# Performance work log

Measured on AMD Instinct MI355X. Metric: run time of the kernel, lower is better.

## Reference

```python
import jax, jax.numpy as jnp
import numpy as np

B, INDIM, POSDIM, L, H, DE, DV, RECEPT = 2, 256, 256, 2048, 8, 64, 64, 64
LN_EPS = 1e-5


def pos_embedding(dim, length):
    # sin/cos with geometric wavelengths length/(0.8 + 1.2**(i+1)); shape (dim, length)
    dsin = dim // 2
    dcos = dim - dsin
    sin_wl = length / (0.8 + 1.2 ** (jnp.arange(dsin, dtype=jnp.float32) + 1.0))[:, None]
    cos_wl = length / (0.8 + 1.2 ** (jnp.arange(dcos, dtype=jnp.float32) + 1.0))[:, None]
    xpos = jnp.arange(length, dtype=jnp.float32)[None, :]
    two_pi = 2.0 * np.pi
    return jnp.concatenate([jnp.sin(two_pi * xpos / sin_wl), jnp.cos(two_pi * xpos / cos_wl)], axis=0)


def _layernorm(x, g, b):
    # normalize over last axis
    mu = jnp.mean(x, axis=-1, keepdims=True)
    var = jnp.mean((x - mu) ** 2, axis=-1, keepdims=True)
    return (x - mu) / jnp.sqrt(var + LN_EPS) * g + b


def setup_inputs() -> dict:
    key = jax.random.key(0)
    ks = jax.random.split(key, 10)
    s = 0.02
    inp = {
        "x": jax.random.normal(ks[0], (B, INDIM, L), dtype=jnp.float32),
        "Wq": jax.random.normal(ks[1], (H * DE, INDIM + POSDIM), dtype=jnp.float32) * s,
        "Wk": jax.random.normal(ks[2], (H * DE, INDIM + POSDIM), dtype=jnp.float32) * s,
        "Wv": jax.random.normal(ks[3], (H * DV, INDIM + POSDIM), dtype=jnp.float32) * s,
        "Wres": jax.random.normal(ks[4], (DV, INDIM), dtype=jnp.float32) * s,
        "Wc": jax.random.normal(ks[5], (DV, H * DV), dtype=jnp.float32) * s,
        "ln1_g": jnp.ones((DV,), jnp.float32),
        "ln1_b": jnp.zeros((DV,), jnp.float32),
        "W1": jax.random.normal(ks[6], (4 * DV, DV), dtype=jnp.float32) * s,
        "W2": jax.random.normal(ks[7], (DV, 4 * DV), dtype=jnp.float32) * s,
        "ln2_g": jnp.ones((DV,), jnp.float32),
        "ln2_b": jnp.zeros((DV,), jnp.float32),
    }
    return inp


def reference(x, Wq, Wk, Wv, Wres, Wc, ln1_g, ln1_b, W1, W2, ln2_g, ln2_b):
    bsz = x.shape[0]
    # residual projection (1x1 conv == channel matmul)
    residual = jnp.einsum('oi,bil->bol', Wres, x)
    # concat positional embedding along channel dim
    pos = pos_embedding(POSDIM, L)
    xp = jnp.concatenate([x, jnp.broadcast_to(pos[None], (bsz,) + pos.shape)], axis=1)
    # QKV projections -> (B, H, D, L)
    q = jnp.einsum('oi,bil->bol', Wq, xp).reshape(bsz, H, DE, L)
    k = jnp.einsum('oi,bil->bol', Wk, xp).reshape(bsz, H, DE, L)
    v = jnp.einsum('oi,bil->bol', Wv, xp).reshape(bsz, H, DV, L)
    # banded receptive attention: mask*(Q^T K); out-of-band scores are exactly 0 (NOT -inf),
    # matching sum(q.unsqueeze(-2) * mask * k.unsqueeze(-3), -1)
    idx = jnp.arange(L)
    band = (jnp.abs(idx[:, None] - idx[None, :]) <= RECEPT).astype(x.dtype)  # (L, L)
    scores = jnp.einsum('bhdl,bhdm->bhlm', q, k) * band / np.float32(np.sqrt(DE))
    attn = jax.nn.softmax(scores, axis=-1)
    # attn @ V^T, back to (B, H, DV, L), flatten heads
    out = jnp.einsum('bhlm,bhvm->bhvl', attn, v).reshape(bsz, H * DV, L)
    pred = jnp.einsum('oi,bil->bol', Wc, out) + residual
    pred = _layernorm(pred.transpose(0, 2, 1), ln1_g, ln1_b).transpose(0, 2, 1)
    # feedforward (1x1 convs) with exact GELU + residual + layernorm
    res2 = pred
    h = jax.nn.gelu(jnp.einsum('oi,bil->bol', W1, pred), approximate=False)
    pred = jnp.einsum('oi,bil->bol', W2, h) + res2
    pred = _layernorm(pred.transpose(0, 2, 1), ln2_g, ln2_b).transpose(0, 2, 1)
    return pred
```

## Files before the change

kernel.cpp:

```cpp
#include <hip/hip_runtime.h>
#include <cstdint>
#include <cstddef>

#define SEQLEN 2048
#define NBATCH 2
#define NIND   256
#define NPOS   256
#define NCIN   512
#define NH     8
#define NDE    64
#define NDV    64
#define NREC   64

typedef __attribute__((ext_vector_type(8))) short s16x8;
typedef __attribute__((ext_vector_type(4))) float f32x4;

__device__ __forceinline__ unsigned short f2bf(float f) {
  union { float f; unsigned u; } v; v.f = f;
  unsigned r = v.u + 0x7fffu + ((v.u >> 16) & 1u);
  return (unsigned short)(r >> 16);
}

__device__ __forceinline__ void gload16(const unsigned short* g, unsigned short* l) {
  __builtin_amdgcn_global_load_lds(
      (const __attribute__((address_space(1))) unsigned int*)g,
      (__attribute__((address_space(3))) unsigned int*)l, 16, 0, 0);
}

__global__ __launch_bounds__(256) void prep_k(const float* __restrict__ x,
                                              const float* __restrict__ Wq,
                                              const float* __restrict__ Wk,
                                              const float* __restrict__ Wv,
                                              const float* __restrict__ Wc,
                                              const float* __restrict__ Wres,
                                              const float* __restrict__ W1,
                                              const float* __restrict__ W2,
                                              unsigned short* __restrict__ xpt,
                                              unsigned short* __restrict__ wqb,
                                              unsigned short* __restrict__ wkb,
                                              unsigned short* __restrict__ wvb,
                                              unsigned short* __restrict__ wcb,
                                              unsigned short* __restrict__ wresb,
                                              unsigned short* __restrict__ w1b,
                                              unsigned short* __restrict__ w2b,
                                              float* __restrict__ vsum) {
  __shared__ float tile[64][65];
  int blk = blockIdx.x;
  int t = threadIdx.x;
  if (blk < 512) {
    int b = blk >> 8, c0 = ((blk >> 5) & 7) * 64, l0 = (blk & 31) * 64;
    if (c0 < NIND) {
      const float* src = x + ((size_t)b * NIND + c0) * SEQLEN;
      int ll = t & 63, cq = t >> 6;
#pragma unroll
      for (int i = 0; i < 16; ++i) {
        int cl = cq * 16 + i;
        tile[cl][ll] = src[(size_t)cl * SEQLEN + l0 + ll];
      }
      __syncthreads();
      int cl2 = t & 63, lq = t >> 6;
      unsigned short* dst = xpt + ((size_t)b * SEQLEN + l0) * NCIN + c0;
#pragma unroll
      for (int i = 0; i < 16; ++i) {
        int l = lq * 16 + i;
        dst[(size_t)l * NCIN + cl2] = f2bf(tile[cl2][l]);
      }
    } else {
      if (b == 1) return;
      int c = c0 + (t & 63);
      int j = c - NIND;
      int i = (j < NPOS / 2) ? j : j - NPOS / 2;
      const double base = (double)1.2f;
      double p = 1.0;
      for (int tt = 0; tt <= i; ++tt) p *= base;
      float w = 0.8f + (float)p;
      float swl = (float)SEQLEN / w;
      const float two_pi = (float)(2.0 * 3.14159265358979323846);
      int wv = t >> 6;
      unsigned short* dst0 = xpt;
      unsigned short* dst1 = xpt + (size_t)SEQLEN * NCIN;
#pragma unroll
      for (int it = 0; it < 16; ++it) {
        int l = l0 + 16 * wv + it;
        float arg = (two_pi * (float)l) / swl;
        unsigned short val = f2bf((j < NPOS / 2) ? sinf(arg) : cosf(arg));
        dst0[(size_t)l * NCIN + c] = val;
        dst1[(size_t)l * NCIN + c] = val;
      }
    }
  } else if (blk == 1360) {
    ((float4*)vsum)[t] = make_float4(0.f, 0.f, 0.f, 0.f);
  } else {
    const float* in;
    unsigned short* out;
    int idx4;
    if (blk < 1280) {
      int i = (blk - 512) * 256 + t;
      int which = i >> 16;
      idx4 = i & 65535;
      in = (which == 0) ? Wq : ((which == 1) ? Wk : Wv);
      out = (which == 0) ? wqb : ((which == 1) ? wkb : wvb);
    } else if (blk < 1312) { in = Wc;   out = wcb;   idx4 = (blk - 1280) * 256 + t; }
    else if (blk < 1328)   { in = Wres; out = wresb; idx4 = (blk - 1312) * 256 + t; }
    else if (blk < 1344)   { in = W1;   out = w1b;   idx4 = (blk - 1328) * 256 + t; }
    else                   { in = W2;   out = w2b;   idx4 = (blk - 1344) * 256 + t; }
    float4 v = ((const float4*)in)[idx4];
    ((ushort4*)out)[idx4] = make_ushort4(f2bf(v.x), f2bf(v.y), f2bf(v.z), f2bf(v.w));
  }
}

__global__ __launch_bounds__(256) void qkv_gemm_k(const unsigned short* __restrict__ Wqb,
                                                  const unsigned short* __restrict__ Wkb,
                                                  const unsigned short* __restrict__ Wvb,
                                                  const unsigned short* __restrict__ xpt,
                                                  unsigned short* __restrict__ qt,
                                                  unsigned short* __restrict__ kt,
                                                  unsigned short* __restrict__ vb,
                                                  float* __restrict__ vsum) {
  __shared__ alignas(16) unsigned short lds[24576];

  int bz = blockIdx.z;
  int y = blockIdx.y;
  int ysel = y >> 3;
  int m0 = (y & 7) * 64;
  int n0 = blockIdx.x * 128;
  const unsigned short* W = (ysel == 0) ? Wqb : ((ysel == 1) ? Wkb : Wvb);
  const unsigned short* Bg = xpt + (size_t)bz * SEQLEN * NCIN;

  int t = threadIdx.x;
  int w = t >> 6, lane = t & 63, lr = lane & 15, hi = lane >> 4;
  int wm = w >> 1, wn = w & 1;

  int sr = lane >> 3;
  int scs = ((lane & 7) ^ sr) * 8;
  const unsigned short* gA0 = W  + (size_t)(m0 + 16 * w + sr) * 512 + scs;
  const unsigned short* gB0 = Bg + (size_t)(n0 + 32 * w + sr) * 512 + scs;

  int swz = (lr & 7) << 3;

  f32x4 acc[2][4];
#pragma unroll
  for (int i = 0; i < 2; ++i)
#pragma unroll
    for (int j = 0; j < 4; ++j) acc[i][j] = (f32x4){0.f, 0.f, 0.f, 0.f};

  auto stage = [&](int buf, int k0) {
    unsigned short* Ad = lds + buf * 12288 + (16 * w) * 64;
    unsigned short* Bd = lds + buf * 12288 + 4096 + (32 * w) * 64;
    gload16(gA0 + k0,            Ad);
    gload16(gA0 + k0 + 8 * 512,  Ad + 8 * 64);
    gload16(gB0 + k0,            Bd);
    gload16(gB0 + k0 + 8 * 512,  Bd + 8 * 64);
    gload16(gB0 + k0 + 16 * 512, Bd + 16 * 64);
    gload16(gB0 + k0 + 24 * 512, Bd + 24 * 64);
  };
  auto compute = [&](int buf) {
    const unsigned short* Ar = lds + buf * 12288;
    const unsigned short* Br = Ar + 4096;
#pragma unroll
    for (int ks = 0; ks < 2; ++ks) {
      s16x8 af[2], bfv[4];
#pragma unroll
      for (int mt = 0; mt < 2; ++mt)
        af[mt] = *(const s16x8*)&Ar[(32 * wm + 16 * mt + lr) * 64 + ((32 * ks + 8 * hi) ^ swz)];
#pragma unroll
      for (int nt = 0; nt < 4; ++nt)
        bfv[nt] = *(const s16x8*)&Br[(64 * wn + 16 * nt + lr) * 64 + ((32 * ks + 8 * hi) ^ swz)];
#pragma unroll
      for (int mt = 0; mt < 2; ++mt)
#pragma unroll
        for (int nt = 0; nt < 4; ++nt)
          acc[mt][nt] = __builtin_amdgcn_mfma_f32_16x16x32_bf16(af[mt], bfv[nt], acc[mt][nt], 0, 0, 0);
    }
  };

  stage(0, 0);
  stage(1, 64);
#pragma unroll
  for (int it = 0; it < 8; ++it) {
    if (it < 7) {
      asm volatile("s_waitcnt vmcnt(6)" ::: "memory");
    } else {
      asm volatile("s_waitcnt vmcnt(0)" ::: "memory");
    }
    __builtin_amdgcn_s_barrier();
    compute(it & 1);
    __builtin_amdgcn_s_barrier();
    if (it < 6) stage(it & 1, (it + 2) * 64);
  }
  __syncthreads();

  if (ysel == 2) {
#pragma unroll
    for (int mt = 0; mt < 2; ++mt)
#pragma unroll
      for (int reg = 0; reg < 4; ++reg) {
        float p = acc[mt][0][reg] + acc[mt][1][reg] + acc[mt][2][reg] + acc[mt][3][reg];
        p += __shfl_xor(p, 1, 64);
        p += __shfl_xor(p, 2, 64);
        p += __shfl_xor(p, 4, 64);
        p += __shfl_xor(p, 8, 64);
        if (lr == 0)
          atomicAdd(&vsum[bz * 512 + m0 + 32 * wm + 16 * mt + 4 * hi + reg], p);
      }
  }

  if (ysel < 2) {
    unsigned short* Cl = lds;
#pragma unroll
    for (int mt = 0; mt < 2; ++mt)
#pragma unroll
      for (int nt = 0; nt < 4; ++nt) {
        int lloc = 64 * wn + 16 * nt + lr;
        int d0 = 32 * wm + 16 * mt + 4 * hi;
        *(ushort4*)&Cl[lloc * 68 + d0] = make_ushort4(f2bf(acc[mt][nt][0]), f2bf(acc[mt][nt][1]),
                                                      f2bf(acc[mt][nt][2]), f2bf(acc[mt][nt][3]));
      }
    __syncthreads();
    int h = m0 >> 6;
    unsigned short* Cb = ((ysel == 0) ? qt : kt) + ((size_t)(bz * NH + h) * SEQLEN + n0) * 64;
    int rr = t >> 1, cc = (t & 1) * 32;
#pragma unroll
    for (int j = 0; j < 4; ++j)
      *(int4*)&Cb[(size_t)rr * 64 + cc + 8 * j] = *(const int4*)&Cl[rr * 68 + cc + 8 * j];
  } else {
    unsigned short* Cl2 = lds;
#pragma unroll
    for (int mt = 0; mt < 2; ++mt)
#pragma unroll
      for (int nt = 0; nt < 4; ++nt) {
        int lloc = 64 * wn + 16 * nt + lr;
#pragma unroll
        for (int reg = 0; reg < 4; ++reg)
          Cl2[(32 * wm + 16 * mt + 4 * hi + reg) * 132 + lloc] = f2bf(acc[mt][nt][reg]);
      }
    __syncthreads();
    int dd = t >> 2, cc = (t & 3) * 32;
    unsigned short* Vb = vb + ((size_t)(bz * 512 + m0 + dd)) * SEQLEN + n0;
#pragma unroll
    for (int j = 0; j < 4; ++j)
      *(int4*)&Vb[cc + 8 * j] = *(const int4*)&Cl2[dd * 132 + cc + 8 * j];
  }
}

__global__ __launch_bounds__(64) void attn_k(const unsigned short* __restrict__ qt,
                                             const unsigned short* __restrict__ kt,
                                             const unsigned short* __restrict__ vb,
                                             const float* __restrict__ vsum,
                                             unsigned short* __restrict__ attnt) {
  __shared__ alignas(16) unsigned short Ps[16][168];
  __shared__ float rowcoef[16];

  int bz = blockIdx.z, hh = blockIdx.y;
  int l0 = blockIdx.x * 16;
  int bh = bz * NH + hh;
  const unsigned short* Qb = qt + (size_t)bh * SEQLEN * 64;
  const unsigned short* Kb = kt + (size_t)bh * SEQLEN * 64;
  const unsigned short* Vp = vb + (size_t)(bz * 512 + hh * 64) * SEQLEN;
  int vsbase = bz * 512 + hh * 64;

  int t = threadIdx.x;
  int lr = t & 15, hi = t >> 4;

  s16x8 a0 = *(const s16x8*)(Qb + ((size_t)(l0 + lr)) * 64 + 8 * hi);
  s16x8 a1 = *(const s16x8*)(Qb + ((size_t)(l0 + lr)) * 64 + 32 + 8 * hi);

  f32x4 sc[9];
#pragma unroll
  for (int ct = 0; ct < 9; ++ct) {
    int m = l0 - 64 + 16 * ct + lr;
    const unsigned short* kp = Kb + (ptrdiff_t)m * 64;
    s16x8 b0 = *(const s16x8*)(kp + 8 * hi);
    s16x8 b1 = *(const s16x8*)(kp + 32 + 8 * hi);
    f32x4 acc = {0.f, 0.f, 0.f, 0.f};
    acc = __builtin_amdgcn_mfma_f32_16x16x32_bf16(a0, b0, acc, 0, 0, 0);
    acc = __builtin_amdgcn_mfma_f32_16x16x32_bf16(a1, b1, acc, 0, 0, 0);
    sc[ct] = acc;
  }

  float rcv[4];
#pragma unroll
  for (int i = 0; i < 4; ++i) {
    int r = 4 * hi + i;
    int l = l0 + r;
    float mx = 0.0f;
    float sv[9];
#pragma unroll
    for (int ct = 0; ct < 9; ++ct) {
      int c = 16 * ct + lr;
      int m = l0 - 64 + c;
      bool ib = (c >= r) && (c <= r + 128) && (m >= 0) && (m < SEQLEN);
      float s = sc[ct][i] * 0.125f;
      sv[ct] = ib ? s : -1e30f;
      mx = ib ? fmaxf(mx, s) : mx;
    }
    mx = fmaxf(mx, __shfl_xor(mx, 1, 64));
    mx = fmaxf(mx, __shfl_xor(mx, 2, 64));
    mx = fmaxf(mx, __shfl_xor(mx, 4, 64));
    mx = fmaxf(mx, __shfl_xor(mx, 8, 64));
    float e0 = expf(-mx);
    float zs = 0.f;
#pragma unroll
    for (int ct = 0; ct < 9; ++ct) {
      float e = (sv[ct] > -1e29f) ? expf(sv[ct] - mx) : 0.0f;
      sv[ct] = e;
      zs += e;
    }
    zs += __shfl_xor(zs, 1, 64);
    zs += __shfl_xor(zs, 2, 64);
    zs += __shfl_xor(zs, 4, 64);
    zs += __shfl_xor(zs, 8, 64);
    int lo = l - NREC; if (lo < 0) lo = 0;
    int hi2 = l + NREC; if (hi2 > SEQLEN - 1) hi2 = SEQLEN - 1;
    float inv = 1.0f / (zs + (float)(SEQLEN - (hi2 - lo + 1)) * e0);
    rcv[i] = e0 * inv;
#pragma unroll
    for (int ct = 0; ct < 9; ++ct)
      sc[ct][i] = (sv[ct] > 0.0f) ? (sv[ct] - e0) * inv : 0.0f;
  }

#pragma unroll
  for (int i = 0; i < 4; ++i) {
    int r = 4 * hi + i;
#pragma unroll
    for (int ct = 0; ct < 9; ++ct)
      Ps[r][16 * ct + lr] = f2bf(sc[ct][i]);
  }
  for (int z = t; z < 16 * 24; z += 64) Ps[z / 24][144 + z % 24] = 0;
  if (lr == 0) {
#pragma unroll
    for (int i = 0; i < 4; ++i) rowcoef[4 * hi + i] = rcv[i];
  }
  __syncthreads();

  float rcf = rowcoef[lr];
  unsigned short* Ob = attnt + ((size_t)bz * SEQLEN + l0 + lr) * 512 + hh * 64;
#pragma unroll
  for (int vt = 0; vt < 4; ++vt) {
    f32x4 acc = {0.f, 0.f, 0.f, 0.f};
#pragma unroll
    for (int ks = 0; ks < 5; ++ks) {
      int m8 = l0 - 64 + 32 * ks + 8 * hi;
      s16x8 av = *(const s16x8*)(Vp + (ptrdiff_t)(16 * vt + lr) * SEQLEN + m8);
      s16x8 b = *(const s16x8*)&Ps[lr][32 * ks + 8 * hi];
      acc = __builtin_amdgcn_mfma_f32_16x16x32_bf16(av, b, acc, 0, 0, 0);
    }
    float vsv[4];
#pragma unroll
    for (int reg = 0; reg < 4; ++reg) vsv[reg] = vsum[vsbase + 16 * vt + 4 * hi + reg];
    ushort4 o = make_ushort4(f2bf(acc[0] + rcf * vsv[0]), f2bf(acc[1] + rcf * vsv[1]),
                             f2bf(acc[2] + rcf * vsv[2]), f2bf(acc[3] + rcf * vsv[3]));
    *(ushort4*)&Ob[16 * vt + 4 * hi] = o;
  }
}

__global__ __launch_bounds__(64) void tail_k(const unsigned short* __restrict__ wcb,
                                             const unsigned short* __restrict__ wresb,
                                             const unsigned short* __restrict__ w1b,
                                             const unsigned short* __restrict__ w2b,
                                             const unsigned short* __restrict__ attnt,
                                             const unsigned short* __restrict__ xpt,
                                             const float* __restrict__ g1v,
                                             const float* __restrict__ b1v,
                                             const float* __restrict__ g2v,
                                             const float* __restrict__ b2v,
                                             float* __restrict__ outp) {
  __shared__ float gs1[64], bs1[64], gs2[64], bs2[64];
  __shared__ alignas(16) unsigned short pw[16][72];
  __shared__ alignas(16) unsigned short hw[16][264];

  int b = blockIdx.y;
  int l0 = blockIdx.x * 16;
  int t = threadIdx.x;
  int lr = t & 15, hi = t >> 4;
  gs1[t] = g1v[t]; bs1[t] = b1v[t]; gs2[t] = g2v[t]; bs2[t] = b2v[t];
  __syncthreads();

  int lloc = lr;
  const unsigned short* brow = attnt + ((size_t)b * SEQLEN + l0 + lloc) * 512;
  const unsigned short* xrow = xpt + ((size_t)b * SEQLEN + l0 + lloc) * 512;

  f32x4 acc[4];
#pragma unroll
  for (int i = 0; i < 4; ++i) acc[i] = (f32x4){0.f, 0.f, 0.f, 0.f};
#pragma unroll
  for (int ks = 0; ks < 16; ++ks) {
    s16x8 bf = *(const s16x8*)(brow + 32 * ks + 8 * hi);
#pragma unroll
    for (int mt = 0; mt < 4; ++mt) {
      s16x8 af = *(const s16x8*)(wcb + (size_t)(16 * mt + lr) * 512 + 32 * ks + 8 * hi);
      acc[mt] = __builtin_amdgcn_mfma_f32_16x16x32_bf16(af, bf, acc[mt], 0, 0, 0);
    }
  }
#pragma unroll
  for (int ks = 0; ks < 8; ++ks) {
    s16x8 bf = *(const s16x8*)(xrow + 32 * ks + 8 * hi);
#pragma unroll
    for (int mt = 0; mt < 4; ++mt) {
      s16x8 af = *(const s16x8*)(wresb + (size_t)(16 * mt + lr) * 256 + 32 * ks + 8 * hi);
      acc[mt] = __builtin_amdgcn_mfma_f32_16x16x32_bf16(af, bf, acc[mt], 0, 0, 0);
    }
  }
  float resid[4][4];
  {
    float sum = 0.f, sq = 0.f;
#pragma unroll
    for (int mt = 0; mt < 4; ++mt)
#pragma unroll
      for (int reg = 0; reg < 4; ++reg) { float v = acc[mt][reg]; sum += v; sq += v * v; }
    sum += __shfl_xor(sum, 16, 64); sq += __shfl_xor(sq, 16, 64);
    sum += __shfl_xor(sum, 32, 64); sq += __shfl_xor(sq, 32, 64);
    float mu = sum * (1.0f / 64.0f);
    float var = sq * (1.0f / 64.0f) - mu * mu;
    float rstd = rsqrtf(var + 1e-5f);
#pragma unroll
    for (int mt = 0; mt < 4; ++mt) {
      float o[4];
#pragma unroll
      for (int reg = 0; reg < 4; ++reg) {
        int m = 16 * mt + 4 * hi + reg;
        o[reg] = (acc[mt][reg] - mu) * rstd * gs1[m] + bs1[m];
        resid[mt][reg] = o[reg];
      }
      *(ushort4*)&pw[lr][16 * mt + 4 * hi] =
          make_ushort4(f2bf(o[0]), f2bf(o[1]), f2bf(o[2]), f2bf(o[3]));
    }
  }
  __syncthreads();

  {
    s16x8 bf0 = *(const s16x8*)&pw[lr][8 * hi];
    s16x8 bf1 = *(const s16x8*)&pw[lr][32 + 8 * hi];
#pragma unroll
    for (int mt = 0; mt < 16; ++mt) {
      s16x8 a0 = *(const s16x8*)(w1b + (size_t)(16 * mt + lr) * 64 + 8 * hi);
      s16x8 a1 = *(const s16x8*)(w1b + (size_t)(16 * mt + lr) * 64 + 32 + 8 * hi);
      f32x4 a2 = {0.f, 0.f, 0.f, 0.f};
      a2 = __builtin_amdgcn_mfma_f32_16x16x32_bf16(a0, bf0, a2, 0, 0, 0);
      a2 = __builtin_amdgcn_mfma_f32_16x16x32_bf16(a1, bf1, a2, 0, 0, 0);
      float v0 = a2[0], v1 = a2[1], v2 = a2[2], v3 = a2[3];
      v0 = 0.5f * v0 * (1.0f + erff(v0 * 0.70710678118654752440f));
      v1 = 0.5f * v1 * (1.0f + erff(v1 * 0.70710678118654752440f));
      v2 = 0.5f * v2 * (1.0f + erff(v2 * 0.70710678118654752440f));
      v3 = 0.5f * v3 * (1.0f + erff(v3 * 0.70710678118654752440f));
      *(ushort4*)&hw[lr][16 * mt + 4 * hi] = make_ushort4(f2bf(v0), f2bf(v1), f2bf(v2), f2bf(v3));
    }
  }
  __syncthreads();

  f32x4 acc3[4];
#pragma unroll
  for (int i = 0; i < 4; ++i) acc3[i] = (f32x4){0.f, 0.f, 0.f, 0.f};
#pragma unroll
  for (int ks = 0; ks < 8; ++ks) {
    s16x8 bf = *(const s16x8*)&hw[lr][32 * ks + 8 * hi];
#pragma unroll
    for (int mt = 0; mt < 4; ++mt) {
      s16x8 af = *(const s16x8*)(w2b + (size_t)(16 * mt + lr) * 256 + 32 * ks + 8 * hi);
      acc3[mt] = __builtin_amdgcn_mfma_f32_16x16x32_bf16(af, bf, acc3[mt], 0, 0, 0);
    }
  }
#pragma unroll
  for (int mt = 0; mt < 4; ++mt)
#pragma unroll
    for (int reg = 0; reg < 4; ++reg) acc3[mt][reg] += resid[mt][reg];
  float sum = 0.f, sq = 0.f;
#pragma unroll
  for (int mt = 0; mt < 4; ++mt)
#pragma unroll
    for (int reg = 0; reg < 4; ++reg) { float v = acc3[mt][reg]; sum += v; sq += v * v; }
  sum += __shfl_xor(sum, 16, 64); sq += __shfl_xor(sq, 16, 64);
  sum += __shfl_xor(sum, 32, 64); sq += __shfl_xor(sq, 32, 64);
  float mu = sum * (1.0f / 64.0f);
  float var = sq * (1.0f / 64.0f) - mu * mu;
  float rstd = rsqrtf(var + 1e-5f);
  float* ob = outp + (size_t)b * 64 * SEQLEN;
  int l = l0 + lloc;
#pragma unroll
  for (int mt = 0; mt < 4; ++mt)
#pragma unroll
    for (int reg = 0; reg < 4; ++reg) {
      int m = 16 * mt + 4 * hi + reg;
      ob[(size_t)m * SEQLEN + l] = (acc3[mt][reg] - mu) * rstd * gs2[m] + bs2[m];
    }
}

extern "C" void kernel_launch(void* const* d_in, const int* in_sizes, int n_in,
                              void* d_out, int out_size, void* d_ws, size_t ws_size,
                              hipStream_t stream) {
  const float* x    = (const float*)d_in[0];
  const float* Wq   = (const float*)d_in[1];
  const float* Wk   = (const float*)d_in[2];
  const float* Wv   = (const float*)d_in[3];
  const float* Wres = (const float*)d_in[4];
  const float* Wc   = (const float*)d_in[5];
  const float* ln1g = (const float*)d_in[6];
  const float* ln1b = (const float*)d_in[7];
  const float* W1   = (const float*)d_in[8];
  const float* W2   = (const float*)d_in[9];
  const float* ln2g = (const float*)d_in[10];
  const float* ln2b = (const float*)d_in[11];

  char* base = (char*)d_ws;
  unsigned short* xpt   = (unsigned short*)base; base += (size_t)2097152 * 2;
  unsigned short* wqb   = (unsigned short*)base; base += (size_t)262144 * 2;
  unsigned short* wkb   = (unsigned short*)base; base += (size_t)262144 * 2;
  unsigned short* wvb   = (unsigned short*)base; base += (size_t)262144 * 2;
  unsigned short* wcb   = (unsigned short*)base; base += (size_t)32768 * 2;
  unsigned short* wresb = (unsigned short*)base; base += (size_t)16384 * 2;
  unsigned short* w1b   = (unsigned short*)base; base += (size_t)16384 * 2;
  unsigned short* w2b   = (unsigned short*)base; base += (size_t)16384 * 2;
  unsigned short* qt    = (unsigned short*)base; base += (size_t)2097152 * 2;
  unsigned short* kt    = (unsigned short*)base; base += (size_t)2097152 * 2;
  unsigned short* vbb   = (unsigned short*)base; base += (size_t)2097152 * 2;
  float* vsum           = (float*)base;          base += (size_t)1024 * 4;
  unsigned short* attnt = (unsigned short*)base; base += (size_t)2097152 * 2;
  float* outp = (float*)d_out;

  prep_k<<<1361, 256, 0, stream>>>(x, Wq, Wk, Wv, Wc, Wres, W1, W2,
                                   xpt, wqb, wkb, wvb, wcb, wresb, w1b, w2b, vsum);
  qkv_gemm_k<<<dim3(16, 24, NBATCH), 256, 0, stream>>>(wqb, wkb, wvb, xpt, qt, kt, vbb, vsum);
  attn_k<<<dim3(128, NH, NBATCH), 64, 0, stream>>>(qt, kt, vbb, vsum, attnt);
  tail_k<<<dim3(128, NBATCH), 64, 0, stream>>>(wcb, wresb, w1b, w2b, attnt, xpt,
                                               ln1g, ln1b, ln2g, ln2b, outp);
}
```

Before: 70.61 us.

## Fuse attention and tail kernels into one cooperative launch with grid sync

Merges the banded attention kernel and the tail projection/FFN/LayerNorm kernel into a single cooperative kernel. Persistent blocks loop over the attention units and then over the tail units, with a grid-wide barrier between the two phases. The aim is to remove one kernel launch and the inter-kernel gap. In exchange it adds grid-sync overhead and limits the grid to the occupancy-derived block count, with the old two-kernel path kept as a fallback if the cooperative launch fails.

```diff
diff --git a/kernel.cpp b/kernel.cpp
--- a/kernel.cpp
+++ b/kernel.cpp
@@ -1,6 +1,9 @@
 #include <hip/hip_runtime.h>
+#include <hip/hip_cooperative_groups.h>
 #include <cstdint>
 #include <cstddef>
+
+namespace cg = cooperative_groups;
 
 #define SEQLEN 2048
 #define NBATCH 2
@@ -243,23 +246,22 @@
   }
 }
 
-__global__ __launch_bounds__(64) void attn_k(const unsigned short* __restrict__ qt,
-                                             const unsigned short* __restrict__ kt,
-                                             const unsigned short* __restrict__ vb,
-                                             const float* __restrict__ vsum,
-                                             unsigned short* __restrict__ attnt) {
-  __shared__ alignas(16) unsigned short Ps[16][168];
-  __shared__ float rowcoef[16];
-
-  int bz = blockIdx.z, hh = blockIdx.y;
-  int l0 = blockIdx.x * 16;
+
+__device__ __forceinline__ void attn_unit_w(
+    int u, int t, void* smem,
+    const unsigned short* qt, const unsigned short* kt,
+    const unsigned short* vb, const float* vsum, unsigned short* attnt) {
+  unsigned short (*Ps)[168] = (unsigned short(*)[168])smem;
+  float* rowcoef = (float*)((char*)smem + 5376);
+
+  int bz = u >> 10, hh = (u >> 7) & 7;
+  int l0 = (u & 127) * 16;
   int bh = bz * NH + hh;
   const unsigned short* Qb = qt + (size_t)bh * SEQLEN * 64;
   const unsigned short* Kb = kt + (size_t)bh * SEQLEN * 64;
   const unsigned short* Vp = vb + (size_t)(bz * 512 + hh * 64) * SEQLEN;
   int vsbase = bz * 512 + hh * 64;
 
-  int t = threadIdx.x;
   int lr = t & 15, hi = t >> 4;
 
   s16x8 a0 = *(const s16x8*)(Qb + ((size_t)(l0 + lr)) * 64 + 8 * hi);
@@ -354,31 +356,28 @@
   }
 }
 
-__global__ __launch_bounds__(64) void tail_k(const unsigned short* __restrict__ wcb,
-                                             const unsigned short* __restrict__ wresb,
-                                             const unsigned short* __restrict__ w1b,
-                                             const unsigned short* __restrict__ w2b,
-                                             const unsigned short* __restrict__ attnt,
-                                             const unsigned short* __restrict__ xpt,
-                                             const float* __restrict__ g1v,
-                                             const float* __restrict__ b1v,
-                                             const float* __restrict__ g2v,
-                                             const float* __restrict__ b2v,
-                                             float* __restrict__ outp) {
-  __shared__ float gs1[64], bs1[64], gs2[64], bs2[64];
-  __shared__ alignas(16) unsigned short pw[16][72];
-  __shared__ alignas(16) unsigned short hw[16][264];
-
-  int b = blockIdx.y;
-  int l0 = blockIdx.x * 16;
-  int t = threadIdx.x;
+__device__ __forceinline__ void tail_unit_w(
+    int u, int t, void* smem,
+    const unsigned short* wcb, const unsigned short* wresb,
+    const unsigned short* w1b, const unsigned short* w2b,
+    const unsigned short* attnt, const unsigned short* xpt,
+    const float* g1v, const float* b1v, const float* g2v, const float* b2v,
+    float* outp) {
+  float* gs1 = (float*)smem;
+  float* bs1 = gs1 + 64;
+  float* gs2 = bs1 + 64;
+  float* bs2 = gs2 + 64;
+  unsigned short (*pw)[72]  = (unsigned short(*)[72])((char*)smem + 1024);
+  unsigned short (*hw)[264] = (unsigned short(*)[264])((char*)smem + 3328);
+
+  int b = u >> 7;
+  int l0 = (u & 127) * 16;
   int lr = t & 15, hi = t >> 4;
   gs1[t] = g1v[t]; bs1[t] = b1v[t]; gs2[t] = g2v[t]; bs2[t] = b2v[t];
   __syncthreads();
 
-  int lloc = lr;
-  const unsigned short* brow = attnt + ((size_t)b * SEQLEN + l0 + lloc) * 512;
-  const unsigned short* xrow = xpt + ((size_t)b * SEQLEN + l0 + lloc) * 512;
+  const unsigned short* brow = attnt + ((size_t)b * SEQLEN + l0 + lr) * 512;
+  const unsigned short* xrow = xpt + ((size_t)b * SEQLEN + l0 + lr) * 512;
 
   f32x4 acc[4];
 #pragma unroll
@@ -475,7 +474,7 @@
   float var = sq * (1.0f / 64.0f) - mu * mu;
   float rstd = rsqrtf(var + 1e-5f);
   float* ob = outp + (size_t)b * 64 * SEQLEN;
-  int l = l0 + lloc;
+  int l = l0 + lr;
 #pragma unroll
   for (int mt = 0; mt < 4; ++mt)
 #pragma unroll
@@ -483,6 +482,62 @@
       int m = 16 * mt + 4 * hi + reg;
       ob[(size_t)m * SEQLEN + l] = (acc3[mt][reg] - mu) * rstd * gs2[m] + bs2[m];
     }
+}
+
+__global__ __launch_bounds__(64) void attn_tail_k(
+    const unsigned short* __restrict__ qt, const unsigned short* __restrict__ kt,
+    const unsigned short* __restrict__ vb, const float* __restrict__ vsum,
+    unsigned short* __restrict__ attnt,
+    const unsigned short* __restrict__ wcb, const unsigned short* __restrict__ wresb,
+    const unsigned short* __restrict__ w1b, const unsigned short* __restrict__ w2b,
+    const unsigned short* __restrict__ xpt,
+    const float* __restrict__ g1v, const float* __restrict__ b1v,
+    const float* __restrict__ g2v, const float* __restrict__ b2v,
+    float* __restrict__ outp) {
+  __shared__ alignas(16) unsigned char smem[11776];
+  int t = threadIdx.x;
+  int bid = blockIdx.x, nb = gridDim.x;
+
+  for (int u = bid; u < 2048; u += nb) {
+    __syncthreads();
+    attn_unit_w(u, t, smem, qt, kt, vb, vsum, attnt);
+  }
+  __threadfence();
+  cg::this_grid().sync();
+  __threadfence();
+
+  for (int u = bid; u < NBATCH * 128; u += nb) {
+    __syncthreads();
+    tail_unit_w(u, t, smem, wcb, wresb, w1b, w2b, attnt, xpt,
+                g1v, b1v, g2v, b2v, outp);
+  }
+}
+
+__global__ __launch_bounds__(64) void attn_k(const unsigned short* __restrict__ qt,
+                                             const unsigned short* __restrict__ kt,
+                                             const unsigned short* __restrict__ vb,
+                                             const float* __restrict__ vsum,
+                                             unsigned short* __restrict__ attnt) {
+  __shared__ alignas(16) unsigned char smem[5440];
+  int u = ((blockIdx.z * NH + blockIdx.y) << 7) | blockIdx.x;
+  attn_unit_w(u, threadIdx.x, smem, qt, kt, vb, vsum, attnt);
+}
+
+__global__ __launch_bounds__(64) void tail_k(const unsigned short* __restrict__ wcb,
+                                             const unsigned short* __restrict__ wresb,
+                                             const unsigned short* __restrict__ w1b,
+                                             const unsigned short* __restrict__ w2b,
+                                             const unsigned short* __restrict__ attnt,
+                                             const unsigned short* __restrict__ xpt,
+                                             const float* __restrict__ g1v,
+                                             const float* __restrict__ b1v,
+                                             const float* __restrict__ g2v,
+                                             const float* __restrict__ b2v,
+                                             float* __restrict__ outp) {
+  __shared__ alignas(16) unsigned char smem[11776];
+  int u = (blockIdx.y << 7) | blockIdx.x;
+  tail_unit_w(u, threadIdx.x, smem, wcb, wresb, w1b, w2b, attnt, xpt,
+              g1v, b1v, g2v, b2v, outp);
 }
 
 extern "C" void kernel_launch(void* const* d_in, const int* in_sizes, int n_in,
@@ -520,7 +575,25 @@
   prep_k<<<1361, 256, 0, stream>>>(x, Wq, Wk, Wv, Wc, Wres, W1, W2,
                                    xpt, wqb, wkb, wvb, wcb, wresb, w1b, w2b, vsum);
   qkv_gemm_k<<<dim3(16, 24, NBATCH), 256, 0, stream>>>(wqb, wkb, wvb, xpt, qt, kt, vbb, vsum);
-  attn_k<<<dim3(128, NH, NBATCH), 64, 0, stream>>>(qt, kt, vbb, vsum, attnt);
-  tail_k<<<dim3(128, NBATCH), 64, 0, stream>>>(wcb, wresb, w1b, w2b, attnt, xpt,
-                                               ln1g, ln1b, ln2g, ln2b, outp);
-}
+
+  int maxb = 0;
+  hipError_t qerr = hipOccupancyMaxActiveBlocksPerMultiprocessor(&maxb, attn_tail_k, 64, 0);
+  int grid = 0;
+  if (qerr == hipSuccess && maxb > 0) {
+    grid = maxb * 256;
+    if (grid > 2048) grid = 2048;
+  }
+  hipError_t lerr = hipErrorUnknown;
+  if (grid > 0) {
+    void* args[] = {(void*)&qt, (void*)&kt, (void*)&vbb, (void*)&vsum, (void*)&attnt,
+                    (void*)&wcb, (void*)&wresb, (void*)&w1b, (void*)&w2b, (void*)&xpt,
+                    (void*)&ln1g, (void*)&ln1b, (void*)&ln2g, (void*)&ln2b, (void*)&outp};
+    lerr = hipLaunchCooperativeKernel((const void*)attn_tail_k, dim3(grid), dim3(64),
+                                      args, 0, stream);
+  }
+  if (lerr != hipSuccess) {
+    attn_k<<<dim3(128, NH, NBATCH), 64, 0, stream>>>(qt, kt, vbb, vsum, attnt);
+    tail_k<<<dim3(128, NBATCH), 64, 0, stream>>>(wcb, wresb, w1b, w2b, attnt, xpt,
+                                                 ln1g, ln1b, ln2g, ln2b, outp);
+  }
+}
```

New measurement: 72.66 us. 1.03x slower.

## Fuse banded attention into tail kernel, keep per-tile attention output in LDS

Applied to the files above, without the earlier changes.

Merges the attention kernel and the output-projection/FFN tail kernel into a single kernel. Each 16-position block loops over all 8 heads and writes the attention output into a shared-memory tile, which then feeds the Wc projection directly. This removes one kernel launch and the round trip of the attention output through global memory. In exchange, the attention grid drops from 2048 single-wave blocks to 256, and each block processes the heads serially. That cuts the parallelism and latency hiding available to the attention phase.

```diff
diff --git a/kernel.cpp b/kernel.cpp
--- a/kernel.cpp
+++ b/kernel.cpp
@@ -243,149 +243,136 @@
   }
 }
 
-__global__ __launch_bounds__(64) void attn_k(const unsigned short* __restrict__ qt,
-                                             const unsigned short* __restrict__ kt,
-                                             const unsigned short* __restrict__ vb,
-                                             const float* __restrict__ vsum,
-                                             unsigned short* __restrict__ attnt) {
+#define ALP 520
+__global__ __launch_bounds__(64) void attn_tail_k(
+    const unsigned short* __restrict__ qt, const unsigned short* __restrict__ kt,
+    const unsigned short* __restrict__ vb, const float* __restrict__ vsum,
+    const unsigned short* __restrict__ wcb, const unsigned short* __restrict__ wresb,
+    const unsigned short* __restrict__ w1b, const unsigned short* __restrict__ w2b,
+    const unsigned short* __restrict__ xpt,
+    const float* __restrict__ g1v, const float* __restrict__ b1v,
+    const float* __restrict__ g2v, const float* __restrict__ b2v,
+    float* __restrict__ outp) {
+  __shared__ alignas(16) unsigned short attn_loc[16][ALP];
   __shared__ alignas(16) unsigned short Ps[16][168];
   __shared__ float rowcoef[16];
-
-  int bz = blockIdx.z, hh = blockIdx.y;
-  int l0 = blockIdx.x * 16;
-  int bh = bz * NH + hh;
-  const unsigned short* Qb = qt + (size_t)bh * SEQLEN * 64;
-  const unsigned short* Kb = kt + (size_t)bh * SEQLEN * 64;
-  const unsigned short* Vp = vb + (size_t)(bz * 512 + hh * 64) * SEQLEN;
-  int vsbase = bz * 512 + hh * 64;
-
-  int t = threadIdx.x;
-  int lr = t & 15, hi = t >> 4;
-
-  s16x8 a0 = *(const s16x8*)(Qb + ((size_t)(l0 + lr)) * 64 + 8 * hi);
-  s16x8 a1 = *(const s16x8*)(Qb + ((size_t)(l0 + lr)) * 64 + 32 + 8 * hi);
-
-  f32x4 sc[9];
-#pragma unroll
-  for (int ct = 0; ct < 9; ++ct) {
-    int m = l0 - 64 + 16 * ct + lr;
-    const unsigned short* kp = Kb + (ptrdiff_t)m * 64;
-    s16x8 b0 = *(const s16x8*)(kp + 8 * hi);
-    s16x8 b1 = *(const s16x8*)(kp + 32 + 8 * hi);
-    f32x4 acc = {0.f, 0.f, 0.f, 0.f};
-    acc = __builtin_amdgcn_mfma_f32_16x16x32_bf16(a0, b0, acc, 0, 0, 0);
-    acc = __builtin_amdgcn_mfma_f32_16x16x32_bf16(a1, b1, acc, 0, 0, 0);
-    sc[ct] = acc;
-  }
-
-  float rcv[4];
-#pragma unroll
-  for (int i = 0; i < 4; ++i) {
-    int r = 4 * hi + i;
-    int l = l0 + r;
-    float mx = 0.0f;
-    float sv[9];
-#pragma unroll
-    for (int ct = 0; ct < 9; ++ct) {
-      int c = 16 * ct + lr;
-      int m = l0 - 64 + c;
-      bool ib = (c >= r) && (c <= r + 128) && (m >= 0) && (m < SEQLEN);
-      float s = sc[ct][i] * 0.125f;
-      sv[ct] = ib ? s : -1e30f;
-      mx = ib ? fmaxf(mx, s) : mx;
-    }
-    mx = fmaxf(mx, __shfl_xor(mx, 1, 64));
-    mx = fmaxf(mx, __shfl_xor(mx, 2, 64));
-    mx = fmaxf(mx, __shfl_xor(mx, 4, 64));
-    mx = fmaxf(mx, __shfl_xor(mx, 8, 64));
-    float e0 = expf(-mx);
-    float zs = 0.f;
-#pragma unroll
-    for (int ct = 0; ct < 9; ++ct) {
-      float e = (sv[ct] > -1e29f) ? expf(sv[ct] - mx) : 0.0f;
-      sv[ct] = e;
-      zs += e;
-    }
-    zs += __shfl_xor(zs, 1, 64);
-    zs += __shfl_xor(zs, 2, 64);
-    zs += __shfl_xor(zs, 4, 64);
-    zs += __shfl_xor(zs, 8, 64);
-    int lo = l - NREC; if (lo < 0) lo = 0;
-    int hi2 = l + NREC; if (hi2 > SEQLEN - 1) hi2 = SEQLEN - 1;
-    float inv = 1.0f / (zs + (float)(SEQLEN - (hi2 - lo + 1)) * e0);
-    rcv[i] = e0 * inv;
-#pragma unroll
-    for (int ct = 0; ct < 9; ++ct)
-      sc[ct][i] = (sv[ct] > 0.0f) ? (sv[ct] - e0) * inv : 0.0f;
-  }
-
-#pragma unroll
-  for (int i = 0; i < 4; ++i) {
-    int r = 4 * hi + i;
-#pragma unroll
-    for (int ct = 0; ct < 9; ++ct)
-      Ps[r][16 * ct + lr] = f2bf(sc[ct][i]);
-  }
-  for (int z = t; z < 16 * 24; z += 64) Ps[z / 24][144 + z % 24] = 0;
-  if (lr == 0) {
-#pragma unroll
-    for (int i = 0; i < 4; ++i) rowcoef[4 * hi + i] = rcv[i];
-  }
-  __syncthreads();
-
-  float rcf = rowcoef[lr];
-  unsigned short* Ob = attnt + ((size_t)bz * SEQLEN + l0 + lr) * 512 + hh * 64;
-#pragma unroll
-  for (int vt = 0; vt < 4; ++vt) {
-    f32x4 acc = {0.f, 0.f, 0.f, 0.f};
-#pragma unroll
-    for (int ks = 0; ks < 5; ++ks) {
-      int m8 = l0 - 64 + 32 * ks + 8 * hi;
-      s16x8 av = *(const s16x8*)(Vp + (ptrdiff_t)(16 * vt + lr) * SEQLEN + m8);
-      s16x8 b = *(const s16x8*)&Ps[lr][32 * ks + 8 * hi];
-      acc = __builtin_amdgcn_mfma_f32_16x16x32_bf16(av, b, acc, 0, 0, 0);
-    }
-    float vsv[4];
-#pragma unroll
-    for (int reg = 0; reg < 4; ++reg) vsv[reg] = vsum[vsbase + 16 * vt + 4 * hi + reg];
-    ushort4 o = make_ushort4(f2bf(acc[0] + rcf * vsv[0]), f2bf(acc[1] + rcf * vsv[1]),
-                             f2bf(acc[2] + rcf * vsv[2]), f2bf(acc[3] + rcf * vsv[3]));
-    *(ushort4*)&Ob[16 * vt + 4 * hi] = o;
-  }
-}
-
-__global__ __launch_bounds__(64) void tail_k(const unsigned short* __restrict__ wcb,
-                                             const unsigned short* __restrict__ wresb,
-                                             const unsigned short* __restrict__ w1b,
-                                             const unsigned short* __restrict__ w2b,
-                                             const unsigned short* __restrict__ attnt,
-                                             const unsigned short* __restrict__ xpt,
-                                             const float* __restrict__ g1v,
-                                             const float* __restrict__ b1v,
-                                             const float* __restrict__ g2v,
-                                             const float* __restrict__ b2v,
-                                             float* __restrict__ outp) {
-  __shared__ float gs1[64], bs1[64], gs2[64], bs2[64];
   __shared__ alignas(16) unsigned short pw[16][72];
   __shared__ alignas(16) unsigned short hw[16][264];
+  __shared__ float gs1[64], bs1[64], gs2[64], bs2[64];
 
   int b = blockIdx.y;
   int l0 = blockIdx.x * 16;
   int t = threadIdx.x;
   int lr = t & 15, hi = t >> 4;
+
   gs1[t] = g1v[t]; bs1[t] = b1v[t]; gs2[t] = g2v[t]; bs2[t] = b2v[t];
-  __syncthreads();
-
-  int lloc = lr;
-  const unsigned short* brow = attnt + ((size_t)b * SEQLEN + l0 + lloc) * 512;
-  const unsigned short* xrow = xpt + ((size_t)b * SEQLEN + l0 + lloc) * 512;
+
+  for (int h = 0; h < NH; ++h) {
+    const unsigned short* Qb = qt + (size_t)(b * NH + h) * SEQLEN * 64;
+    const unsigned short* Kb = kt + (size_t)(b * NH + h) * SEQLEN * 64;
+    const unsigned short* Vp = vb + (size_t)(b * 512 + h * 64) * SEQLEN;
+    int vsbase = b * 512 + h * 64;
+
+    s16x8 a0 = *(const s16x8*)(Qb + ((size_t)(l0 + lr)) * 64 + 8 * hi);
+    s16x8 a1 = *(const s16x8*)(Qb + ((size_t)(l0 + lr)) * 64 + 32 + 8 * hi);
+
+    f32x4 sc[9];
+#pragma unroll
+    for (int ct = 0; ct < 9; ++ct) {
+      int m = l0 - 64 + 16 * ct + lr;
+      const unsigned short* kp = Kb + (ptrdiff_t)m * 64;
+      s16x8 b0 = *(const s16x8*)(kp + 8 * hi);
+      s16x8 b1 = *(const s16x8*)(kp + 32 + 8 * hi);
+      f32x4 acc = {0.f, 0.f, 0.f, 0.f};
+      acc = __builtin_amdgcn_mfma_f32_16x16x32_bf16(a0, b0, acc, 0, 0, 0);
+      acc = __builtin_amdgcn_mfma_f32_16x16x32_bf16(a1, b1, acc, 0, 0, 0);
+      sc[ct] = acc;
+    }
+
+    float rcv[4];
+#pragma unroll
+    for (int i = 0; i < 4; ++i) {
+      int r = 4 * hi + i;
+      int l = l0 + r;
+      float mx = 0.0f;
+      float sv[9];
+#pragma unroll
+      for (int ct = 0; ct < 9; ++ct) {
+        int c = 16 * ct + lr;
+        int m = l0 - 64 + c;
+        bool ib = (c >= r) && (c <= r + 128) && (m >= 0) && (m < SEQLEN);
+        float s = sc[ct][i] * 0.125f;
+        sv[ct] = ib ? s : -1e30f;
+        mx = ib ? fmaxf(mx, s) : mx;
+      }
+      mx = fmaxf(mx, __shfl_xor(mx, 1, 64));
+      mx = fmaxf(mx, __shfl_xor(mx, 2, 64));
+      mx = fmaxf(mx, __shfl_xor(mx, 4, 64));
+      mx = fmaxf(mx, __shfl_xor(mx, 8, 64));
+      float e0 = expf(-mx);
+      float zs = 0.f;
+#pragma unroll
+      for (int ct = 0; ct < 9; ++ct) {
+        float e = (sv[ct] > -1e29f) ? expf(sv[ct] - mx) : 0.0f;
+        sv[ct] = e;
+        zs += e;
+      }
+      zs += __shfl_xor(zs, 1, 64);
+      zs += __shfl_xor(zs, 2, 64);
+      zs += __shfl_xor(zs, 4, 64);
+      zs += __shfl_xor(zs, 8, 64);
+      int lo = l - NREC; if (lo < 0) lo = 0;
+      int hi2 = l + NREC; if (hi2 > SEQLEN - 1) hi2 = SEQLEN - 1;
+      float inv = 1.0f / (zs + (float)(SEQLEN - (hi2 - lo + 1)) * e0);
+      rcv[i] = e0 * inv;
+#pragma unroll
+      for (int ct = 0; ct < 9; ++ct)
+        sc[ct][i] = (sv[ct] > 0.0f) ? (sv[ct] - e0) * inv : 0.0f;
+    }
+
+#pragma unroll
+    for (int i = 0; i < 4; ++i) {
+      int r = 4 * hi + i;
+#pragma unroll
+      for (int ct = 0; ct < 9; ++ct)
+        Ps[r][16 * ct + lr] = f2bf(sc[ct][i]);
+    }
+    for (int z = t; z < 16 * 24; z += 64) Ps[z / 24][144 + z % 24] = 0;
+    if (lr == 0) {
+#pragma unroll
+      for (int i = 0; i < 4; ++i) rowcoef[4 * hi + i] = rcv[i];
+    }
+    __syncthreads();
+
+    float rcf = rowcoef[lr];
+#pragma unroll
+    for (int vt = 0; vt < 4; ++vt) {
+      f32x4 acc = {0.f, 0.f, 0.f, 0.f};
+#pragma unroll
+      for (int ks = 0; ks < 5; ++ks) {
+        int m8 = l0 - 64 + 32 * ks + 8 * hi;
+        s16x8 av = *(const s16x8*)(Vp + (ptrdiff_t)(16 * vt + lr) * SEQLEN + m8);
+        s16x8 bfr = *(const s16x8*)&Ps[lr][32 * ks + 8 * hi];
+        acc = __builtin_amdgcn_mfma_f32_16x16x32_bf16(av, bfr, acc, 0, 0, 0);
+      }
+      float vsv[4];
+#pragma unroll
+      for (int reg = 0; reg < 4; ++reg) vsv[reg] = vsum[vsbase + 16 * vt + 4 * hi + reg];
+      ushort4 o = make_ushort4(f2bf(acc[0] + rcf * vsv[0]), f2bf(acc[1] + rcf * vsv[1]),
+                               f2bf(acc[2] + rcf * vsv[2]), f2bf(acc[3] + rcf * vsv[3]));
+      *(ushort4*)&attn_loc[lr][h * 64 + 16 * vt + 4 * hi] = o;
+    }
+    __syncthreads();
+  }
+
+  const unsigned short* xrow = xpt + ((size_t)b * SEQLEN + l0 + lr) * 512;
 
   f32x4 acc[4];
 #pragma unroll
   for (int i = 0; i < 4; ++i) acc[i] = (f32x4){0.f, 0.f, 0.f, 0.f};
 #pragma unroll
   for (int ks = 0; ks < 16; ++ks) {
-    s16x8 bf = *(const s16x8*)(brow + 32 * ks + 8 * hi);
+    s16x8 bf = *(const s16x8*)&attn_loc[lr][32 * ks + 8 * hi];
 #pragma unroll
     for (int mt = 0; mt < 4; ++mt) {
       s16x8 af = *(const s16x8*)(wcb + (size_t)(16 * mt + lr) * 512 + 32 * ks + 8 * hi);
@@ -475,7 +462,7 @@
   float var = sq * (1.0f / 64.0f) - mu * mu;
   float rstd = rsqrtf(var + 1e-5f);
   float* ob = outp + (size_t)b * 64 * SEQLEN;
-  int l = l0 + lloc;
+  int l = l0 + lr;
 #pragma unroll
   for (int mt = 0; mt < 4; ++mt)
 #pragma unroll
@@ -514,13 +501,12 @@
   unsigned short* kt    = (unsigned short*)base; base += (size_t)2097152 * 2;
   unsigned short* vbb   = (unsigned short*)base; base += (size_t)2097152 * 2;
   float* vsum           = (float*)base;          base += (size_t)1024 * 4;
-  unsigned short* attnt = (unsigned short*)base; base += (size_t)2097152 * 2;
   float* outp = (float*)d_out;
 
   prep_k<<<1361, 256, 0, stream>>>(x, Wq, Wk, Wv, Wc, Wres, W1, W2,
                                    xpt, wqb, wkb, wvb, wcb, wresb, w1b, w2b, vsum);
   qkv_gemm_k<<<dim3(16, 24, NBATCH), 256, 0, stream>>>(wqb, wkb, wvb, xpt, qt, kt, vbb, vsum);
-  attn_k<<<dim3(128, NH, NBATCH), 64, 0, stream>>>(qt, kt, vbb, vsum, attnt);
-  tail_k<<<dim3(128, NBATCH), 64, 0, stream>>>(wcb, wresb, w1b, w2b, attnt, xpt,
-                                               ln1g, ln1b, ln2g, ln2b, outp);
+  attn_tail_k<<<dim3(128, NBATCH), 64, 0, stream>>>(qt, kt, vbb, vsum,
+                                                    wcb, wresb, w1b, w2b, xpt,
+                                                    ln1g, ln1b, ln2g, ln2b, outp);
 }
```

New measurement: 123.1 us. 74.3% more time.
